# Optimization experiments

Hardware: AMD Instinct MI355X
Metric: run time of the kernel (lower is better)

Reference implementation:

```python
import jax, jax.numpy as jnp
import numpy as np

T, B, IN = 64, 4096, 145
H1, H2 = 150, 32


def _lstm_layer(x, w_ih, w_hh, b_ih, b_hh):
    """Single LSTM layer, PyTorch gate order (i, f, g, o).
    x: (T, B, in_dim); w_ih: (4H, in_dim); w_hh: (4H, H); biases: (4H,).
    Returns hidden sequence (T, B, H)."""
    H = w_hh.shape[1]
    Bsz = x.shape[1]
    # Precompute input contribution for all timesteps at once (one big GEMM).
    xg = jnp.einsum('tbi,gi->tbg', x, w_ih) + (b_ih + b_hh)  # (T, B, 4H)
    w_hh_t = w_hh.T  # (H, 4H)

    def step(carry, xg_t):
        h, c = carry
        gates = xg_t + h @ w_hh_t  # (B, 4H)
        i, f, g, o = jnp.split(gates, 4, axis=-1)
        i = jax.nn.sigmoid(i)
        f = jax.nn.sigmoid(f)
        g = jnp.tanh(g)
        o = jax.nn.sigmoid(o)
        c = f * c + i * g
        h = o * jnp.tanh(c)
        return (h, c), h

    h0 = jnp.zeros((Bsz, H), x.dtype)
    c0 = jnp.zeros((Bsz, H), x.dtype)
    _, hs = jax.lax.scan(step, (h0, c0), xg)
    return hs  # (T, B, H)


def _init_lstm_params(key, in_dim, hidden):
    # PyTorch init: U(-k, k) with k = 1/sqrt(hidden)
    k = 1.0 / np.sqrt(hidden)
    ks = jax.random.split(key, 4)
    w_ih = jax.random.uniform(ks[0], (4 * hidden, in_dim), jnp.float32, -k, k)
    w_hh = jax.random.uniform(ks[1], (4 * hidden, hidden), jnp.float32, -k, k)
    b_ih = jax.random.uniform(ks[2], (4 * hidden,), jnp.float32, -k, k)
    b_hh = jax.random.uniform(ks[3], (4 * hidden,), jnp.float32, -k, k)
    return w_ih, w_hh, b_ih, b_hh


def setup_inputs() -> dict:
    key = jax.random.key(0)
    kx, k0, k1, k2 = jax.random.split(key, 4)
    x = jax.random.normal(kx, (T, B, IN), jnp.float32)
    w_ih_l0, w_hh_l0, b_ih_l0, b_hh_l0 = _init_lstm_params(k0, IN, H1)
    w_ih_l1, w_hh_l1, b_ih_l1, b_hh_l1 = _init_lstm_params(k1, H1, H1)
    w_ih_l2, w_hh_l2, b_ih_l2, b_hh_l2 = _init_lstm_params(k2, H1, H2)
    return {
        'x': x,
        'w_ih_l0': w_ih_l0, 'w_hh_l0': w_hh_l0, 'b_ih_l0': b_ih_l0, 'b_hh_l0': b_hh_l0,
        'w_ih_l1': w_ih_l1, 'w_hh_l1': w_hh_l1, 'b_ih_l1': b_ih_l1, 'b_hh_l1': b_hh_l1,
        'w_ih_l2': w_ih_l2, 'w_hh_l2': w_hh_l2, 'b_ih_l2': b_ih_l2, 'b_hh_l2': b_hh_l2,
    }


def reference(x,
              w_ih_l0, w_hh_l0, b_ih_l0, b_hh_l0,
              w_ih_l1, w_hh_l1, b_ih_l1, b_hh_l1,
              w_ih_l2, w_hh_l2, b_ih_l2, b_hh_l2):
    # temporal_model1: 2-layer LSTM (145 -> 150 -> 150)
    h = _lstm_layer(x, w_ih_l0, w_hh_l0, b_ih_l0, b_hh_l0)
    h = _lstm_layer(h, w_ih_l1, w_hh_l1, b_ih_l1, b_hh_l1)
    # temporal_model2: 1-layer LSTM (150 -> 32)
    out2 = _lstm_layer(h, w_ih_l2, w_hh_l2, b_ih_l2, b_hh_l2)
    return out2  # (T, B, 32)
```

## Files before the change

kernel.cpp:

```cpp
#include <hip/hip_runtime.h>


typedef _Float16 f16;
typedef _Float16 f16x8 __attribute__((ext_vector_type(8)));
typedef _Float16 f16x4 __attribute__((ext_vector_type(4)));
typedef float f32x4 __attribute__((ext_vector_type(4)));

#define T_STEPS 64
#define BATCH 4096

__device__ __forceinline__ float fexp(float x) {
  return __builtin_amdgcn_exp2f(x * 1.44269504088896340736f);
}
__device__ __forceinline__ float sigf(float x) {
  return __builtin_amdgcn_rcpf(1.0f + fexp(-x));
}
__device__ __forceinline__ float tanh_f(float x) {
  return 1.0f - 2.0f * __builtin_amdgcn_rcpf(1.0f + fexp(2.0f * x));
}

#define BAR_LGKM() asm volatile("s_waitcnt lgkmcnt(0)\n\ts_barrier" ::: "memory")

__global__ __launch_bounds__(256) void prep_w(
    const float* __restrict__ wih0, const float* __restrict__ bih0, const float* __restrict__ bhh0,
    const float* __restrict__ wih1, const float* __restrict__ bih1, const float* __restrict__ bhh1,
    f16* __restrict__ wprep0, f16* __restrict__ wprep1,
    float* __restrict__ bias0, float* __restrict__ bias1) {
  int idx = blockIdx.x * 256 + threadIdx.x;
  constexpr int WE = 640 * 168;
  if (idx < WE) {
    int c = idx / 168, k = idx - c * 168;
    int gate = c / 160, cg = c - gate * 160;
    float v = (cg < 150 && k < 145) ? wih0[(size_t)(gate * 150 + cg) * 145 + k] : 0.f;
    wprep0[idx] = (f16)v;
  } else if (idx < 2 * WE) {
    int e = idx - WE;
    int c = e / 168, k = e - c * 168;
    int gate = c / 160, cg = c - gate * 160;
    float v = (cg < 150 && k < 150) ? wih1[(size_t)(gate * 150 + cg) * 150 + k] : 0.f;
    wprep1[e] = (f16)v;
  } else if (idx < 2 * WE + 640) {
    int c = idx - 2 * WE;
    int gate = c / 160, cg = c - gate * 160;
    bias0[c] = (cg < 150) ? (bih0[gate * 150 + cg] + bhh0[gate * 150 + cg]) : 0.f;
  } else if (idx < 2 * WE + 1280) {
    int c = idx - 2 * WE - 640;
    int gate = c / 160, cg = c - gate * 160;
    bias1[c] = (cg < 150) ? (bih1[gate * 150 + cg] + bhh1[gate * 150 + cg]) : 0.f;
  }
}

template <int IN_DIM, int SRC_F16>
__global__ __launch_bounds__(512, 4) void gemm_xg2(
    const float* __restrict__ xin_f32, const f16* __restrict__ xin_f16,
    const f16* __restrict__ wprep, const float* __restrict__ bias_pre,
    f16* __restrict__ xg) {
  constexpr int ASTR = 168;
  __shared__ __align__(16) f16 A_lds[128 * ASTR];
  __shared__ __align__(16) f16 W_lds[64 * ASTR];
  __shared__ __align__(16) float bias_lds[640];
  const int tid = threadIdx.x;
  const int mtile = blockIdx.x;
  const int g0 = mtile * 128;

  if constexpr (SRC_F16) {
    const f16* src = xin_f16 + (size_t)g0 * ASTR;
#pragma unroll
    for (int q = 0; q < 6; ++q) {
      int i = q * 512 + tid;
      if (i < 2688) *(f16x8*)(&A_lds[i * 8]) = *(const f16x8*)(src + (size_t)i * 8);
    }
  } else {
#pragma unroll
    for (int q = 0; q < 42; ++q) {
      int idx = q * 512 + tid;
      int r = idx / ASTR, c = idx - r * ASTR;
      float v = (c < IN_DIM) ? xin_f32[(size_t)(g0 + r) * IN_DIM + c] : 0.f;
      A_lds[idx] = (f16)v;
    }
  }
  if (tid < 160) *(f32x4*)(&bias_lds[tid * 4]) = *(const f32x4*)(bias_pre + tid * 4);
#pragma unroll
  for (int q = 0; q < 3; ++q) {
    int i = q * 512 + tid;
    if (i < 1344) *(f16x8*)(&W_lds[i * 8]) = *(const f16x8*)(wprep + (size_t)i * 8);
  }
  __syncthreads();

  const int l = tid & 63, wv = tid >> 6;
  const int p = wv >> 1, cq = wv & 1;
  const int lrow = l & 15, lk8 = (l >> 4) * 8, r0 = (l >> 4) * 4;
  const int arow0 = (2 * p) * 16 + lrow;
  const int wrow0 = (2 * cq) * 16 + lrow;

  f16x8 pv0, pv1, pv2;
  for (int ch = 0; ch < 10; ++ch) {
    if (ch < 9) {
      const f16* wsrc = wprep + (size_t)(ch + 1) * 10752;
      pv0 = *(const f16x8*)(wsrc + (size_t)tid * 8);
      pv1 = *(const f16x8*)(wsrc + (size_t)(tid + 512) * 8);
      if (tid < 320) pv2 = *(const f16x8*)(wsrc + (size_t)(tid + 1024) * 8);
    }
    f32x4 a00 = {}, a01 = {}, a10 = {}, a11 = {};
#pragma unroll
    for (int kc = 0; kc < 5; ++kc) {
      f16x8 a0 = *(const f16x8*)(&A_lds[arow0 * ASTR + kc * 32 + lk8]);
      f16x8 a1 = *(const f16x8*)(&A_lds[(arow0 + 16) * ASTR + kc * 32 + lk8]);
      f16x8 b0 = *(const f16x8*)(&W_lds[wrow0 * ASTR + kc * 32 + lk8]);
      f16x8 b1 = *(const f16x8*)(&W_lds[(wrow0 + 16) * ASTR + kc * 32 + lk8]);
      a00 = __builtin_amdgcn_mfma_f32_16x16x32_f16(a0, b0, a00, 0, 0, 0);
      a01 = __builtin_amdgcn_mfma_f32_16x16x32_f16(a0, b1, a01, 0, 0, 0);
      a10 = __builtin_amdgcn_mfma_f32_16x16x32_f16(a1, b0, a10, 0, 0, 0);
      a11 = __builtin_amdgcn_mfma_f32_16x16x32_f16(a1, b1, a11, 0, 0, 0);
    }
    {
      int c0 = ch * 64 + (2 * cq) * 16 + lrow;
      int c1 = c0 + 16;
      float bs0 = bias_lds[c0], bs1 = bias_lds[c1];
      f16x4 o;
      size_t rg0 = (size_t)(mtile * 8 + 2 * p);
#pragma unroll
      for (int j = 0; j < 4; ++j) o[j] = (f16)(a00[j] + bs0);
      *(f16x4*)(xg + (rg0 * 640 + c0) * 16 + r0) = o;
#pragma unroll
      for (int j = 0; j < 4; ++j) o[j] = (f16)(a01[j] + bs1);
      *(f16x4*)(xg + (rg0 * 640 + c1) * 16 + r0) = o;
#pragma unroll
      for (int j = 0; j < 4; ++j) o[j] = (f16)(a10[j] + bs0);
      *(f16x4*)(xg + ((rg0 + 1) * 640 + c0) * 16 + r0) = o;
#pragma unroll
      for (int j = 0; j < 4; ++j) o[j] = (f16)(a11[j] + bs1);
      *(f16x4*)(xg + ((rg0 + 1) * 640 + c1) * 16 + r0) = o;
    }
    if (ch < 9) {
      __syncthreads();
      *(f16x8*)(&W_lds[tid * 8]) = pv0;
      *(f16x8*)(&W_lds[(tid + 512) * 8]) = pv1;
      if (tid < 320) *(f16x8*)(&W_lds[(tid + 1024) * 8]) = pv2;
      __syncthreads();
    }
  }
}

__global__ __launch_bounds__(640, 2) void lstm_rec(
    const f16* __restrict__ xg, const float* __restrict__ whh,
    f16* __restrict__ hout) {
  constexpr int H = 150, HSTR = 168, CPAD = 640;
  __shared__ __align__(16) f16 hbuf[2][16 * HSTR];
  const int tid = threadIdx.x;
  const int l = tid & 63, w = tid >> 6;
  const int lrow = l & 15, lk8 = (l >> 4) * 8, r0 = (l >> 4) * 4;
  const int col = w * 16 + lrow;
  const int bx = blockIdx.x, b0 = bx * 16;

  for (int i = tid; i < 2 * 16 * HSTR / 8; i += 640) {
    f16x8 z = {};
    *(f16x8*)(&hbuf[0][0] + (size_t)i * 8) = z;
  }

  f16x8 wh[4][5];
#pragma unroll
  for (int g = 0; g < 4; ++g)
#pragma unroll
    for (int kc = 0; kc < 5; ++kc) {
      f16x8 v;
#pragma unroll
      for (int j = 0; j < 8; ++j) {
        int k = kc * 32 + lk8 + j;
        float x = (col < H && k < H) ? whh[((size_t)g * H + col) * H + k] : 0.f;
        v[j] = (f16)x;
      }
      wh[g][kc] = v;
    }
  __syncthreads();

  float creg[4] = {0.f, 0.f, 0.f, 0.f};
  f16x4 pv[4];
#pragma unroll
  for (int g = 0; g < 4; ++g)
    pv[g] = *(const f16x4*)(xg + ((size_t)bx * CPAD + g * 160 + col) * 16 + r0);

  for (int t = 0; t < T_STEPS; ++t) {
    const int cur = t & 1, nxt = cur ^ 1;

    f32x4 acc[4];
#pragma unroll
    for (int g = 0; g < 4; ++g) {
#pragma unroll
      for (int j = 0; j < 4; ++j) acc[g][j] = (float)pv[g][j];
    }
    if (t + 1 < T_STEPS) {
#pragma unroll
      for (int g = 0; g < 4; ++g)
        pv[g] = *(const f16x4*)(xg + ((size_t)((t + 1) * 256 + bx) * CPAD + g * 160 + col) * 16 + r0);
    }
    if (t > 0 && tid < 336) {
      f16x8 v = *(const f16x8*)(&hbuf[cur][tid * 8]);
      *(f16x8*)(hout + ((size_t)(t - 1) * BATCH + b0) * 168 + (size_t)tid * 8) = v;
    }

#pragma unroll
    for (int kc = 0; kc < 5; ++kc) {
      f16x8 a = *(const f16x8*)(&hbuf[cur][lrow * HSTR + kc * 32 + lk8]);
#pragma unroll
      for (int g = 0; g < 4; ++g)
        acc[g] = __builtin_amdgcn_mfma_f32_16x16x32_f16(a, wh[g][kc], acc[g], 0, 0, 0);
    }

#pragma unroll
    for (int j = 0; j < 4; ++j) {
      float iv = sigf(acc[0][j]);
      float fv = sigf(acc[1][j]);
      float gv = tanh_f(acc[2][j]);
      float ov = sigf(acc[3][j]);
      float c = fv * creg[j] + iv * gv;
      creg[j] = c;
      float h = ov * tanh_f(c);
      hbuf[nxt][(r0 + j) * HSTR + col] = (f16)h;
    }

    BAR_LGKM();
  }
  if (tid < 336) {
    f16x8 v = *(const f16x8*)(&hbuf[0][tid * 8]);
    *(f16x8*)(hout + ((size_t)(T_STEPS - 1) * BATCH + b0) * 168 + (size_t)tid * 8) = v;
  }
}

template <int IN_DIM, int H, int MODE>
__global__ __launch_bounds__(512, 2) void lstm_layer(
    const float* __restrict__ xin_f32, const f16* __restrict__ xin_f16,
    const float* __restrict__ w_ih, const float* __restrict__ w_hh,
    const float* __restrict__ b_ih, const float* __restrict__ b_hh,
    f16* __restrict__ hout, float* __restrict__ yout) {
  constexpr int KX = (IN_DIM + 31) / 32;
  constexpr int XSTR = KX * 32 + 8;
  constexpr int KH = (H + 31) / 32;
  constexpr int HSTR = KH * 32 + 8;
  constexpr int NPAD = ((H + 31) / 32) * 32;
  constexpr int NT = NPAD / 32;
  constexpr int GROUPS = NPAD * 4;
  constexpr int UPD_ITERS = (GROUPS + 511) / 512;
  constexpr int XIN_ELEMS = 16 * IN_DIM;
  constexpr int QX = (XIN_ELEMS + 511) / 512;
  constexpr int STG = (16 * XSTR) / 8;
  constexpr int HCP = (16 * HSTR) / 8;
  static_assert(MODE == 0 || XSTR == 168, "");

  __shared__ __align__(16) f16 xbuf[2][16 * XSTR];
  __shared__ __align__(16) f16 hbuf[16 * HSTR];
  __shared__ __align__(16) float gates[NPAD * 84];

  const int tid = threadIdx.x;
  const int l = tid & 63;
  const int wv = tid >> 6;
  const int gate = wv >> 1;
  const int half = wv & 1;
  const int lrow = l & 15;
  const int lk8 = (l >> 4) * 8;
  const int r0 = (l >> 4) * 4;
  const int b0 = blockIdx.x * 16;

  {
    f16* xf = &xbuf[0][0];
    for (int i = tid; i < 2 * 16 * XSTR; i += 512) xf[i] = (f16)0.f;
    for (int i = tid; i < 16 * HSTR; i += 512) hbuf[i] = (f16)0.f;
  }
  const int rbase = half * (NPAD / 2) + lrow;
  float bias_reg[NT];
#pragma unroll
  for (int nt = 0; nt < NT; ++nt) {
    int n = rbase + nt * 16;
    bias_reg[nt] = (n < H) ? (b_ih[gate * H + n] + b_hh[gate * H + n]) : 0.f;
  }
  f16x8 wx[KX][NT], wh[KH][NT];
#pragma unroll
  for (int kc = 0; kc < KX; ++kc)
#pragma unroll
    for (int nt = 0; nt < NT; ++nt) {
      f16x8 wq;
#pragma unroll
      for (int j = 0; j < 8; ++j) {
        int k = kc * 32 + lk8 + j;
        int r = rbase + nt * 16;
        float v = (r < H && k < IN_DIM) ? w_ih[(size_t)(gate * H + r) * IN_DIM + k] : 0.f;
        wq[j] = (f16)v;
      }
      wx[kc][nt] = wq;
    }
#pragma unroll
  for (int kc = 0; kc < KH; ++kc)
#pragma unroll
    for (int nt = 0; nt < NT; ++nt) {
      f16x8 wq;
#pragma unroll
      for (int j = 0; j < 8; ++j) {
        int k = kc * 32 + lk8 + j;
        int r = rbase + nt * 16;
        float v = (r < H && k < H) ? w_hh[(size_t)(gate * H + r) * H + k] : 0.f;
        wq[j] = (f16)v;
      }
      wh[kc][nt] = wq;
    }

  if constexpr (MODE == 0) {
#pragma unroll
    for (int q = 0; q < QX; ++q) {
      int idx = q * 512 + tid;
      if (idx < XIN_ELEMS) {
        float v = xin_f32[(size_t)b0 * IN_DIM + idx];
        int r = idx / IN_DIM, c = idx - r * IN_DIM;
        xbuf[0][r * XSTR + c] = (f16)v;
      }
    }
  } else {
    if (tid < STG) {
      f16x8 v = *(const f16x8*)(xin_f16 + (size_t)b0 * 168 + tid * 8);
      *(f16x8*)(&xbuf[0][tid * 8]) = v;
    }
  }
  __syncthreads();

  float creg[UPD_ITERS][4];
#pragma unroll
  for (int it = 0; it < UPD_ITERS; ++it)
#pragma unroll
    for (int j = 0; j < 4; ++j) creg[it][j] = 0.f;

  float xv[QX];
  f16x8 pv;

  for (int t = 0; t < T_STEPS; ++t) {
    const int cur = t & 1, nxt = cur ^ 1;
    if (t + 1 < T_STEPS) {
      if constexpr (MODE == 0) {
        const float* src = xin_f32 + ((size_t)(t + 1) * BATCH + b0) * IN_DIM;
#pragma unroll
        for (int q = 0; q < QX; ++q) {
          int idx = q * 512 + tid;
          xv[q] = (idx < XIN_ELEMS) ? src[idx] : 0.f;
        }
      } else {
        if (tid < STG)
          pv = *(const f16x8*)(xin_f16 + ((size_t)(t + 1) * BATCH + b0) * 168 + tid * 8);
      }
    }
    if constexpr (MODE != 2) {
      if (t > 0 && tid < HCP) {
        f16x8 v = *(const f16x8*)(&hbuf[tid * 8]);
        *(f16x8*)(hout + ((size_t)(t - 1) * BATCH + b0) * 168 + tid * 8) = v;
      }
    }
    f32x4 acc[NT];
#pragma unroll
    for (int nt = 0; nt < NT; ++nt) {
      float b = bias_reg[nt];
      acc[nt] = f32x4{b, b, b, b};
    }
    {
      const f16* xb = &xbuf[cur][0];
#pragma unroll
      for (int kc = 0; kc < KX; ++kc) {
        f16x8 a = *(const f16x8*)(xb + lrow * XSTR + kc * 32 + lk8);
#pragma unroll
        for (int nt = 0; nt < NT; ++nt)
          acc[nt] = __builtin_amdgcn_mfma_f32_16x16x32_f16(a, wx[kc][nt], acc[nt], 0, 0, 0);
      }
#pragma unroll
      for (int kc = 0; kc < KH; ++kc) {
        f16x8 a = *(const f16x8*)(hbuf + lrow * HSTR + kc * 32 + lk8);
#pragma unroll
        for (int nt = 0; nt < NT; ++nt)
          acc[nt] = __builtin_amdgcn_mfma_f32_16x16x32_f16(a, wh[kc][nt], acc[nt], 0, 0, 0);
      }
    }
#pragma unroll
    for (int nt = 0; nt < NT; ++nt) {
      int n = half * (NPAD / 2) + nt * 16 + lrow;
      *(f32x4*)(&gates[n * 84 + gate * 20 + r0]) = acc[nt];
    }
    BAR_LGKM();
    if (t + 1 < T_STEPS) {
      if constexpr (MODE == 0) {
#pragma unroll
        for (int q = 0; q < QX; ++q) {
          int idx = q * 512 + tid;
          if (idx < XIN_ELEMS) {
            int r = idx / IN_DIM, c = idx - r * IN_DIM;
            xbuf[nxt][r * XSTR + c] = (f16)xv[q];
          }
        }
      } else {
        if (tid < STG) *(f16x8*)(&xbuf[nxt][tid * 8]) = pv;
      }
    }
#pragma unroll
    for (int it = 0; it < UPD_ITERS; ++it) {
      int grp = it * 512 + tid;
      if (grp < GROUPS) {
        int n = grp % NPAD;
        int rb = (grp / NPAD) * 4;
        if (n < H) {
          f32x4 gi = *(const f32x4*)(&gates[n * 84 + 0 + rb]);
          f32x4 gf = *(const f32x4*)(&gates[n * 84 + 20 + rb]);
          f32x4 gg = *(const f32x4*)(&gates[n * 84 + 40 + rb]);
          f32x4 go = *(const f32x4*)(&gates[n * 84 + 60 + rb]);
#pragma unroll
          for (int j = 0; j < 4; ++j) {
            float iv = sigf(gi[j]);
            float fv = sigf(gf[j]);
            float gv = tanh_f(gg[j]);
            float ov = sigf(go[j]);
            float c = fv * creg[it][j] + iv * gv;
            creg[it][j] = c;
            float h = ov * tanh_f(c);
            hbuf[(rb + j) * HSTR + n] = (f16)h;
            if constexpr (MODE == 2) {
              yout[((size_t)t * BATCH + b0 + rb + j) * 32 + n] = h;
            }
          }
        }
      }
    }
    BAR_LGKM();
  }
  if constexpr (MODE != 2) {
    if (tid < HCP) {
      f16x8 v = *(const f16x8*)(&hbuf[tid * 8]);
      *(f16x8*)(hout + ((size_t)(T_STEPS - 1) * BATCH + b0) * 168 + tid * 8) = v;
    }
  }
}

extern "C" void kernel_launch(void* const* d_in, const int* in_sizes, int n_in,
                              void* d_out, int out_size, void* d_ws, size_t ws_size,
                              hipStream_t stream) {
  const float* x = (const float*)d_in[0];
  const float* wih0 = (const float*)d_in[1];
  const float* whh0 = (const float*)d_in[2];
  const float* bih0 = (const float*)d_in[3];
  const float* bhh0 = (const float*)d_in[4];
  const float* wih1 = (const float*)d_in[5];
  const float* whh1 = (const float*)d_in[6];
  const float* bih1 = (const float*)d_in[7];
  const float* bhh1 = (const float*)d_in[8];
  const float* wih2 = (const float*)d_in[9];
  const float* whh2 = (const float*)d_in[10];
  const float* bih2 = (const float*)d_in[11];
  const float* bhh2 = (const float*)d_in[12];

  const size_t HSEQ_BYTES = (size_t)T_STEPS * BATCH * 168 * sizeof(f16);
  const size_t XG_BYTES = (size_t)T_STEPS * BATCH * 640 * sizeof(f16);
  const size_t WPREP_BYTES = (size_t)640 * 168 * sizeof(f16);
  const size_t NEED = HSEQ_BYTES + XG_BYTES + 2 * WPREP_BYTES + 2 * 640 * sizeof(float);
  f16* hws = (f16*)d_ws;
  float* out = (float*)d_out;

  if (ws_size >= NEED) {
    char* base = (char*)d_ws;
    f16* xgbuf = (f16*)(base + HSEQ_BYTES);
    f16* wprep0 = (f16*)(base + HSEQ_BYTES + XG_BYTES);
    f16* wprep1 = (f16*)(base + HSEQ_BYTES + XG_BYTES + WPREP_BYTES);
    float* bias0 = (float*)(base + HSEQ_BYTES + XG_BYTES + 2 * WPREP_BYTES);
    float* bias1 = bias0 + 640;

    prep_w<<<dim3(846), dim3(256), 0, stream>>>(wih0, bih0, bhh0, wih1, bih1, bhh1,
                                                wprep0, wprep1, bias0, bias1);
    dim3 gg(2048), gb(512);
    dim3 rg(BATCH / 16), rb(640);
    gemm_xg2<145, 0><<<gg, gb, 0, stream>>>(x, nullptr, wprep0, bias0, xgbuf);
    lstm_rec<<<rg, rb, 0, stream>>>(xgbuf, whh0, hws);
    gemm_xg2<150, 1><<<gg, gb, 0, stream>>>(nullptr, hws, wprep1, bias1, xgbuf);
    lstm_rec<<<rg, rb, 0, stream>>>(xgbuf, whh1, hws);
    lstm_layer<150, 32, 2><<<dim3(BATCH / 16), dim3(512), 0, stream>>>(
        nullptr, hws, wih2, whh2, bih2, bhh2, nullptr, out);
  } else {
    dim3 grid(BATCH / 16), block(512);
    lstm_layer<145, 150, 0><<<grid, block, 0, stream>>>(x, nullptr, wih0, whh0, bih0, bhh0, hws, nullptr);
    lstm_layer<150, 150, 1><<<grid, block, 0, stream>>>(nullptr, hws, wih1, whh1, bih1, bhh1, hws, nullptr);
    lstm_layer<150, 32, 2><<<grid, block, 0, stream>>>(nullptr, hws, wih2, whh2, bih2, bhh2, nullptr, out);
  }
}
```

Before: 652.1 us.

## Load GEMM weight fragments straight into registers and vectorize fp32 input staging

```diff
diff --git a/kernel.cpp b/kernel.cpp
--- a/kernel.cpp
+++ b/kernel.cpp
@@ -51,94 +51,100 @@
 }
 
 template <int IN_DIM, int SRC_F16>
-__global__ __launch_bounds__(512, 4) void gemm_xg2(
+__global__ __launch_bounds__(512, 2) void gemm_xg3(
     const float* __restrict__ xin_f32, const f16* __restrict__ xin_f16,
     const f16* __restrict__ wprep, const float* __restrict__ bias_pre,
     f16* __restrict__ xg) {
   constexpr int ASTR = 168;
   __shared__ __align__(16) f16 A_lds[128 * ASTR];
-  __shared__ __align__(16) f16 W_lds[64 * ASTR];
   __shared__ __align__(16) float bias_lds[640];
   const int tid = threadIdx.x;
   const int mtile = blockIdx.x;
   const int g0 = mtile * 128;
 
   if constexpr (SRC_F16) {
-    const f16* src = xin_f16 + (size_t)g0 * ASTR;
 #pragma unroll
     for (int q = 0; q < 6; ++q) {
       int i = q * 512 + tid;
-      if (i < 2688) *(f16x8*)(&A_lds[i * 8]) = *(const f16x8*)(src + (size_t)i * 8);
+      if (i < 2688)
+        *(f16x8*)(&A_lds[i * 8]) = *(const f16x8*)(xin_f16 + (size_t)g0 * ASTR + (size_t)i * 8);
     }
   } else {
 #pragma unroll
-    for (int q = 0; q < 42; ++q) {
+    for (int q = 0; q < 10; ++q) {
       int idx = q * 512 + tid;
-      int r = idx / ASTR, c = idx - r * ASTR;
-      float v = (c < IN_DIM) ? xin_f32[(size_t)(g0 + r) * IN_DIM + c] : 0.f;
-      A_lds[idx] = (f16)v;
+      int r = idx / 40, c4 = (idx - r * 40) * 4;
+      f16x4 o;
+      if (c4 + 4 <= IN_DIM) {
+        f32x4 v;
+        __builtin_memcpy(&v, xin_f32 + (size_t)(g0 + r) * IN_DIM + c4, 16);
+#pragma unroll
+        for (int j = 0; j < 4; ++j) o[j] = (f16)v[j];
+      } else {
+#pragma unroll
+        for (int j = 0; j < 4; ++j)
+          o[j] = (c4 + j < IN_DIM) ? (f16)xin_f32[(size_t)(g0 + r) * IN_DIM + c4 + j] : (f16)0.f;
+      }
+      *(f16x4*)(&A_lds[r * ASTR + c4]) = o;
     }
   }
   if (tid < 160) *(f32x4*)(&bias_lds[tid * 4]) = *(const f32x4*)(bias_pre + tid * 4);
-#pragma unroll
-  for (int q = 0; q < 3; ++q) {
-    int i = q * 512 + tid;
-    if (i < 1344) *(f16x8*)(&W_lds[i * 8]) = *(const f16x8*)(wprep + (size_t)i * 8);
-  }
   __syncthreads();
 
   const int l = tid & 63, wv = tid >> 6;
   const int p = wv >> 1, cq = wv & 1;
   const int lrow = l & 15, lk8 = (l >> 4) * 8, r0 = (l >> 4) * 4;
   const int arow0 = (2 * p) * 16 + lrow;
-  const int wrow0 = (2 * cq) * 16 + lrow;
-
-  f16x8 pv0, pv1, pv2;
+  const size_t rg0 = (size_t)(mtile * 8 + 2 * p);
+
+  const f16* wb = wprep + (size_t)(cq * 32 + lrow) * ASTR + lk8;
+
+  f16x8 b0[5], b1[5], n0[5], n1[5];
+#pragma unroll
+  for (int kc = 0; kc < 5; ++kc) {
+    b0[kc] = *(const f16x8*)(wb + kc * 32);
+    b1[kc] = *(const f16x8*)(wb + 16 * ASTR + kc * 32);
+  }
+
   for (int ch = 0; ch < 10; ++ch) {
     if (ch < 9) {
-      const f16* wsrc = wprep + (size_t)(ch + 1) * 10752;
-      pv0 = *(const f16x8*)(wsrc + (size_t)tid * 8);
-      pv1 = *(const f16x8*)(wsrc + (size_t)(tid + 512) * 8);
-      if (tid < 320) pv2 = *(const f16x8*)(wsrc + (size_t)(tid + 1024) * 8);
-    }
-    f32x4 a00 = {}, a01 = {}, a10 = {}, a11 = {};
+      const f16* wn = wb + (size_t)(ch + 1) * 64 * ASTR;
+#pragma unroll
+      for (int kc = 0; kc < 5; ++kc) {
+        n0[kc] = *(const f16x8*)(wn + kc * 32);
+        n1[kc] = *(const f16x8*)(wn + 16 * ASTR + kc * 32);
+      }
+    }
+    const int c0 = ch * 64 + cq * 32 + lrow;
+    const float bs0 = bias_lds[c0], bs1 = bias_lds[c0 + 16];
+    f32x4 a00 = {bs0, bs0, bs0, bs0}, a01 = {bs1, bs1, bs1, bs1};
+    f32x4 a10 = a00, a11 = a01;
 #pragma unroll
     for (int kc = 0; kc < 5; ++kc) {
       f16x8 a0 = *(const f16x8*)(&A_lds[arow0 * ASTR + kc * 32 + lk8]);
       f16x8 a1 = *(const f16x8*)(&A_lds[(arow0 + 16) * ASTR + kc * 32 + lk8]);
-      f16x8 b0 = *(const f16x8*)(&W_lds[wrow0 * ASTR + kc * 32 + lk8]);
-      f16x8 b1 = *(const f16x8*)(&W_lds[(wrow0 + 16) * ASTR + kc * 32 + lk8]);
-      a00 = __builtin_amdgcn_mfma_f32_16x16x32_f16(a0, b0, a00, 0, 0, 0);
-      a01 = __builtin_amdgcn_mfma_f32_16x16x32_f16(a0, b1, a01, 0, 0, 0);
-      a10 = __builtin_amdgcn_mfma_f32_16x16x32_f16(a1, b0, a10, 0, 0, 0);
-      a11 = __builtin_amdgcn_mfma_f32_16x16x32_f16(a1, b1, a11, 0, 0, 0);
+      a00 = __builtin_amdgcn_mfma_f32_16x16x32_f16(a0, b0[kc], a00, 0, 0, 0);
+      a01 = __builtin_amdgcn_mfma_f32_16x16x32_f16(a0, b1[kc], a01, 0, 0, 0);
+      a10 = __builtin_amdgcn_mfma_f32_16x16x32_f16(a1, b0[kc], a10, 0, 0, 0);
+      a11 = __builtin_amdgcn_mfma_f32_16x16x32_f16(a1, b1[kc], a11, 0, 0, 0);
     }
     {
-      int c0 = ch * 64 + (2 * cq) * 16 + lrow;
-      int c1 = c0 + 16;
-      float bs0 = bias_lds[c0], bs1 = bias_lds[c1];
       f16x4 o;
-      size_t rg0 = (size_t)(mtile * 8 + 2 * p);
-#pragma unroll
-      for (int j = 0; j < 4; ++j) o[j] = (f16)(a00[j] + bs0);
+#pragma unroll
+      for (int j = 0; j < 4; ++j) o[j] = (f16)a00[j];
       *(f16x4*)(xg + (rg0 * 640 + c0) * 16 + r0) = o;
 #pragma unroll
-      for (int j = 0; j < 4; ++j) o[j] = (f16)(a01[j] + bs1);
-      *(f16x4*)(xg + (rg0 * 640 + c1) * 16 + r0) = o;
-#pragma unroll
-      for (int j = 0; j < 4; ++j) o[j] = (f16)(a10[j] + bs0);
+      for (int j = 0; j < 4; ++j) o[j] = (f16)a01[j];
+      *(f16x4*)(xg + (rg0 * 640 + c0 + 16) * 16 + r0) = o;
+#pragma unroll
+      for (int j = 0; j < 4; ++j) o[j] = (f16)a10[j];
       *(f16x4*)(xg + ((rg0 + 1) * 640 + c0) * 16 + r0) = o;
 #pragma unroll
-      for (int j = 0; j < 4; ++j) o[j] = (f16)(a11[j] + bs1);
-      *(f16x4*)(xg + ((rg0 + 1) * 640 + c1) * 16 + r0) = o;
-    }
-    if (ch < 9) {
-      __syncthreads();
-      *(f16x8*)(&W_lds[tid * 8]) = pv0;
-      *(f16x8*)(&W_lds[(tid + 512) * 8]) = pv1;
-      if (tid < 320) *(f16x8*)(&W_lds[(tid + 1024) * 8]) = pv2;
-      __syncthreads();
-    }
+      for (int j = 0; j < 4; ++j) o[j] = (f16)a11[j];
+      *(f16x4*)(xg + ((rg0 + 1) * 640 + c0 + 16) * 16 + r0) = o;
+    }
+#pragma unroll
+    for (int kc = 0; kc < 5; ++kc) { b0[kc] = n0[kc]; b1[kc] = n1[kc]; }
   }
 }
 
@@ -468,9 +474,9 @@
                                                 wprep0, wprep1, bias0, bias1);
     dim3 gg(2048), gb(512);
     dim3 rg(BATCH / 16), rb(640);
-    gemm_xg2<145, 0><<<gg, gb, 0, stream>>>(x, nullptr, wprep0, bias0, xgbuf);
+    gemm_xg3<145, 0><<<gg, gb, 0, stream>>>(x, nullptr, wprep0, bias0, xgbuf);
     lstm_rec<<<rg, rb, 0, stream>>>(xgbuf, whh0, hws);
-    gemm_xg2<150, 1><<<gg, gb, 0, stream>>>(nullptr, hws, wprep1, bias1, xgbuf);
+    gemm_xg3<150, 1><<<gg, gb, 0, stream>>>(nullptr, hws, wprep1, bias1, xgbuf);
     lstm_rec<<<rg, rb, 0, stream>>>(xgbuf, whh1, hws);
     lstm_layer<150, 32, 2><<<dim3(BATCH / 16), dim3(512), 0, stream>>>(
         nullptr, hws, wih2, whh2, bih2, bhh2, nullptr, out);
```

Result: slower. 748.9 us (+14.9%).
